# Optimization experiments

Hardware: AMD Instinct MI355X
Metric: run time of the kernel (lower is better)

## Reference

```python
import jax, jax.numpy as jnp
import numpy as np

N = 10000   # num nodes
E = 160000  # num edges (avg degree 16)
B = 8       # batch dim carried on node state
D = 64      # hidden_size


def setup_inputs() -> dict:
    key = jax.random.key(0)
    k1, k2, k3, k4, k5, k6 = jax.random.split(key, 6)
    state = jax.random.normal(k1, (N, B, D), jnp.float32)
    feature = jax.random.normal(k2, (N, 32), jnp.float32)  # unused by GAT math, kept for call signature
    weight = jax.random.normal(k3, (2 * D, D), jnp.float32) * 0.05
    src = jax.random.randint(k4, (E,), 0, N, jnp.int32)
    dst = jax.random.randint(k5, (E,), 0, N, jnp.int32)
    dist = jax.random.uniform(k6, (E, 1), jnp.float32)
    return dict(state=state, feature=feature, weight=weight, src=src, dst=dst, dist=dist)


def reference(state, feature, weight, src, dst, dist):
    # --- msg_edge: gather src/dst node states per edge ---
    src_state = state[src]                 # [E,B,D]
    dst_state = state[dst]                 # [E,B,D]
    es = jnp.concatenate([src_state, dst_state], axis=-1)          # [E,B,2D]
    alpha = jax.nn.leaky_relu(jnp.einsum('ebk,kd->ebd', es, weight),
                              negative_slope=0.2)                  # tf.nn.leaky_relu alpha=0.2
    alpha = alpha * dist[:, :, None]       # dist [E,1] broadcast to [E,1,1]

    # --- msg_reduce: segment softmax over incoming edges of each dst node ---
    amax = jax.ops.segment_max(alpha, dst, num_segments=N)         # [N,B,D]
    ex = jnp.exp(alpha - amax[dst])                                # stable exp
    denom = jax.ops.segment_sum(ex, dst, num_segments=N)           # [N,B,D]
    attn = ex / denom[dst]                                         # [E,B,D]

    # weighted sum of src states scattered back to dst nodes, then relu
    new_state = jax.nn.relu(jax.ops.segment_sum(attn * src_state, dst, num_segments=N))
    return new_state
```

## Files before the change

### kernel.cpp

```cpp
#include <hip/hip_runtime.h>
#include <hip/hip_fp16.h>
#include <math.h>

#define N_NODES 10000
#define N_EDGES 160000
#define B_ 8
#define D_ 64
#define BD 512
#define ROWS 80000
#define SLICE 640000
#define CAP 48

typedef _Float16 f16x8 __attribute__((ext_vector_type(8)));
typedef float f32x4 __attribute__((ext_vector_type(4)));
typedef float f4v __attribute__((ext_vector_type(4)));
typedef unsigned int u32;

union HU { _Float16 f; unsigned short u; };
union HC { u32 u; __half2 h; };

__global__ void __launch_bounds__(256) prep_kernel(
    const int* __restrict__ src, const int* __restrict__ dst,
    const float* __restrict__ dist, int* __restrict__ counts, u32* __restrict__ bucket,
    const float* __restrict__ state, const float* __restrict__ weight,
    __half2* __restrict__ G, __half* __restrict__ Pd) {
    __shared__ _Float16 At[64 * 72];
    __shared__ _Float16 Bt[128 * 72];
    __shared__ u32 Gs[64 * 64];
    __shared__ unsigned short Ps[64 * 64];
    int bid = blockIdx.x;
    int tid = threadIdx.x;

    if (bid < 625) {
        int e = bid * 256 + tid;
        int s = src[e];
        int d = dst[e];
        float di = dist[e];
        int pos = atomicAdd(&counts[d], 1);
        if (pos < CAP) {
            unsigned short hd = __half_as_ushort(__float2half_rn(di * 1.44269504f));
            bucket[d * CAP + pos] = (u32)s | ((u32)hd << 16);
        }
        return;
    }

    int row0 = (bid - 625) * 64;

    const f4v* st4 = (const f4v*)(state + (size_t)row0 * 64);
    for (int i = tid; i < 1024; i += 256) {
        int r = i >> 4, c4 = (i & 15) << 2;
        f4v v = __builtin_nontemporal_load(&st4[i]);
        union { short4 s; _Float16 h[4]; } u;
        u.h[0] = (_Float16)v[0]; u.h[1] = (_Float16)v[1];
        u.h[2] = (_Float16)v[2]; u.h[3] = (_Float16)v[3];
        *(short4*)&At[r * 72 + c4] = u.s;
    }
    const f4v* w4 = (const f4v*)weight;
    for (int i = tid; i < 2048; i += 256) {
        int r = i >> 4, c4 = (i & 15) << 2;
        f4v v = w4[i];
        int h = r >> 6, k = r & 63;
        int nb = h * 64 + c4;
        Bt[(nb + 0) * 72 + k] = (_Float16)v[0];
        Bt[(nb + 1) * 72 + k] = (_Float16)v[1];
        Bt[(nb + 2) * 72 + k] = (_Float16)v[2];
        Bt[(nb + 3) * 72 + k] = (_Float16)v[3];
    }
    __syncthreads();

    int wave = tid >> 6, lane = tid & 63;
    int quad = lane >> 4, m16 = lane & 15;
    int m_loc = wave * 16 + m16;

    f16x8 a0 = *(const f16x8*)&At[m_loc * 72 + quad * 8];
    f16x8 a1 = *(const f16x8*)&At[m_loc * 72 + 32 + quad * 8];

#pragma unroll
    for (int tcol = 0; tcol < 8; tcol++) {
        int n = tcol * 16 + m16;
        f16x8 b0 = *(const f16x8*)&Bt[n * 72 + quad * 8];
        f16x8 b1 = *(const f16x8*)&Bt[n * 72 + 32 + quad * 8];
        f32x4 acc = {0.f, 0.f, 0.f, 0.f};
        acc = __builtin_amdgcn_mfma_f32_16x16x32_f16(a0, b0, acc, 0, 0, 0);
        acc = __builtin_amdgcn_mfma_f32_16x16x32_f16(a1, b1, acc, 0, 0, 0);
#pragma unroll
        for (int r = 0; r < 4; r++) {
            int ml = wave * 16 + quad * 4 + r;
            if (tcol < 4) {
                HU xu; xu.f = At[ml * 72 + n];
                Gs[ml * 64 + n] = (u32)__half_as_ushort(__float2half_rn(acc[r]))
                                  | ((u32)xu.u << 16);
            } else {
                Ps[ml * 64 + (n - 64)] = __half_as_ushort(__float2half_rn(acc[r]));
            }
        }
    }
    __syncthreads();

    for (int i = tid; i < 1024; i += 256) {
        int row = i >> 4, seg = i & 15;
        int m = row0 + row;
        size_t base = (size_t)(m & 7) * SLICE + (size_t)(m >> 3) * 64;
        *(float4*)&G[base + seg * 4] = *(const float4*)&Gs[row * 64 + seg * 4];
    }
    for (int i = tid; i < 512; i += 256) {
        int row = i >> 3, seg = i & 7;
        int m = row0 + row;
        size_t base = (size_t)(m & 7) * SLICE + (size_t)(m >> 3) * 64;
        *(float4*)&Pd[base + seg * 8] = *(const float4*)&Ps[row * 64 + seg * 8];
    }
}

__global__ void __launch_bounds__(256) gat_aggregate(
    const __half2* __restrict__ G,
    const __half* __restrict__ Pds,
    const int* __restrict__ counts,
    const u32* __restrict__ bucket,
    float* __restrict__ out) {
    int bid = blockIdx.x;
    int b = bid & 7;
    int grp = bid >> 3;
    int wave = threadIdx.x >> 6;
    int lane = threadIdx.x & 63;
    int n = (grp << 2) + wave;
    int eidx = lane >> 4;
    int lpart = lane & 15;

    const __half2* Gb = G + (size_t)b * SLICE;
    const __half* Pb = Pds + (size_t)b * SLICE;

    union { double d; __half2 h[2]; } pdu;
    pdu.d = *(const double*)(Pb + n * 64 + lpart * 4);
    __half2 pd01 = pdu.h[0], pd23 = pdu.h[1];

    int cnt = counts[n];
    if (cnt > CAP) cnt = CAP;
    const u32* ep = bucket + n * CAP;

    const __half2 c06 = __float2half2_rn(0.6f);
    const __half2 c04 = __float2half2_rn(0.4f);
    const u32 ABSM = 0x7fff7fffu;

    __half2 l01 = __float2half2_rn(0.f), l23 = l01;
    __half2 o01 = l01, o23 = l01;

    if (cnt > 0) {
        int last = cnt - 1;
        int iA = eidx <= last ? eidx : last;
        int iB = (4 + eidx) <= last ? (4 + eidx) : last;
        u32 recA = ep[iA];
        u32 recB = ep[iB];
        float4 gA = *(const float4*)(Gb + (size_t)(recA & 0xffffu) * 64 + lpart * 4);
        float4 gB = *(const float4*)(Gb + (size_t)(recB & 0xffffu) * 64 + lpart * 4);
        __half hA = __ushort_as_half((unsigned short)(recA >> 16));
        __half hB = __ushort_as_half((unsigned short)(recB >> 16));
        __half2 dA = __halves2half2(hA, hA);
        __half2 dB = __halves2half2(hB, hB);

        int j = 0;
        for (;;) {
            int jn = j + 8;
            bool more = jn < cnt;
            float4 gA2, gB2; __half2 dA2, dB2;
            if (more) {
                int a2 = jn + eidx;      a2 = a2 <= last ? a2 : last;
                int b2 = jn + 4 + eidx;  b2 = b2 <= last ? b2 : last;
                u32 rA2 = ep[a2];
                u32 rB2 = ep[b2];
                gA2 = *(const float4*)(Gb + (size_t)(rA2 & 0xffffu) * 64 + lpart * 4);
                gB2 = *(const float4*)(Gb + (size_t)(rB2 & 0xffffu) * 64 + lpart * 4);
                __half h2a = __ushort_as_half((unsigned short)(rA2 >> 16));
                __half h2b = __ushort_as_half((unsigned short)(rB2 >> 16));
                dA2 = __halves2half2(h2a, h2a);
                dB2 = __halves2half2(h2b, h2b);
            }
#pragma unroll
            for (int c = 0; c < 2; c++) {
                bool act = (j + c * 4 + eidx) <= last;
                float4 g = c == 0 ? gA : gB;
                __half2 ddl = c == 0 ? dA : dB;
                union { float4 f; __half2 h[4]; } gu; gu.f = g;
                __half2 p01 = __halves2half2(__low2half(gu.h[0]), __low2half(gu.h[1]));
                __half2 p23 = __halves2half2(__low2half(gu.h[2]), __low2half(gu.h[3]));
                __half2 x01 = __halves2half2(__high2half(gu.h[0]), __high2half(gu.h[1]));
                __half2 x23 = __halves2half2(__high2half(gu.h[2]), __high2half(gu.h[3]));
                __half2 z01 = __hadd2(p01, pd01);
                __half2 z23 = __hadd2(p23, pd23);
                HC az01, az23, zz01, zz23;
                zz01.h = z01; zz23.h = z23;
                az01.u = zz01.u & ABSM;
                az23.u = zz23.u & ABSM;
                __half2 lk01 = __hfma2(az01.h, c04, __hmul2(z01, c06));
                __half2 lk23 = __hfma2(az23.h, c04, __hmul2(z23, c06));
                __half2 a01 = __hmul2(lk01, ddl);
                __half2 a23 = __hmul2(lk23, ddl);
                __half2 e01 = __halves2half2(hexp2(__low2half(a01)), hexp2(__high2half(a01)));
                __half2 e23 = __halves2half2(hexp2(__low2half(a23)), hexp2(__high2half(a23)));
                HC s01, s23;
                s01.h = e01; s23.h = e23;
                s01.u = act ? s01.u : 0u;
                s23.u = act ? s23.u : 0u;
                l01 = __hadd2(l01, s01.h);
                l23 = __hadd2(l23, s23.h);
                o01 = __hfma2(s01.h, x01, o01);
                o23 = __hfma2(s23.h, x23, o23);
            }
            if (!more) break;
            j = jn; gA = gA2; gB = gB2; dA = dA2; dB = dB2;
        }
#pragma unroll
        for (int m = 16; m <= 32; m <<= 1) {
            HC c;
            c.u = (u32)__shfl_xor((int)((HC){.h = l01}).u, m, 64); l01 = __hadd2(l01, c.h);
            c.u = (u32)__shfl_xor((int)((HC){.h = l23}).u, m, 64); l23 = __hadd2(l23, c.h);
            c.u = (u32)__shfl_xor((int)((HC){.h = o01}).u, m, 64); o01 = __hadd2(o01, c.h);
            c.u = (u32)__shfl_xor((int)((HC){.h = o23}).u, m, 64); o23 = __hadd2(o23, c.h);
        }
    }
    if (eidx == 0) {
        float4 r;
        if (cnt > 0) {
            float l0 = __low2float(l01), l1 = __high2float(l01);
            float l2 = __low2float(l23), l3 = __high2float(l23);
            float o0 = __low2float(o01), o1 = __high2float(o01);
            float o2 = __low2float(o23), o3 = __high2float(o23);
            r.x = fmaxf(o0 * __builtin_amdgcn_rcpf(l0), 0.f);
            r.y = fmaxf(o1 * __builtin_amdgcn_rcpf(l1), 0.f);
            r.z = fmaxf(o2 * __builtin_amdgcn_rcpf(l2), 0.f);
            r.w = fmaxf(o3 * __builtin_amdgcn_rcpf(l3), 0.f);
        } else {
            r = make_float4(0.f, 0.f, 0.f, 0.f);
        }
        *(float4*)(out + (size_t)n * BD + b * 64 + lpart * 4) = r;
    }
}

extern "C" void kernel_launch(void* const* d_in, const int* in_sizes, int n_in,
                              void* d_out, int out_size, void* d_ws, size_t ws_size,
                              hipStream_t stream) {
    const float* state  = (const float*)d_in[0];
    const float* weight = (const float*)d_in[2];
    const int*   src    = (const int*)d_in[3];
    const int*   dst    = (const int*)d_in[4];
    const float* dist   = (const float*)d_in[5];

    __half2* G      = (__half2*)d_ws;
    __half*  Pd     = (__half*)(G + (size_t)8 * SLICE);
    u32*     bucket = (u32*)(Pd + (size_t)8 * SLICE);
    int*     counts = (int*)(bucket + (size_t)N_NODES * CAP);

    hipMemsetAsync(counts, 0, N_NODES * sizeof(int), stream);
    prep_kernel<<<1875, 256, 0, stream>>>(src, dst, dist, counts, bucket,
                                          state, weight, G, Pd);
    gat_aggregate<<<N_NODES * 2, 256, 0, stream>>>(G, Pd, counts, bucket, (float*)d_out);
}
```

Baseline: 155.1 us.

## Pad edge buckets with zero records and repack G as separate p/x half2 pairs

Edge buckets are widened to a padded stride and zeroed by the memset. The aggregate loop now runs over a count rounded up to a multiple of 8, with no per-edge clamping or masking. The padding edges' contribution (node 0, zero dist, so exp=1) is subtracted afterwards. G is also repacked so that the projection halves and the state halves are contiguous half2 pairs, which removes the per-edge shuffling of halves. The cost is a larger memset and an fp16 correction that may lose precision.

```diff
diff --git a/kernel.cpp b/kernel.cpp
--- a/kernel.cpp
+++ b/kernel.cpp
@@ -10,6 +10,7 @@
 #define ROWS 80000
 #define SLICE 640000
 #define CAP 48
+#define CAPR 56
 
 typedef _Float16 f16x8 __attribute__((ext_vector_type(8)));
 typedef float f32x4 __attribute__((ext_vector_type(4)));
@@ -23,10 +24,10 @@
     const int* __restrict__ src, const int* __restrict__ dst,
     const float* __restrict__ dist, int* __restrict__ counts, u32* __restrict__ bucket,
     const float* __restrict__ state, const float* __restrict__ weight,
-    __half2* __restrict__ G, __half* __restrict__ Pd) {
+    u32* __restrict__ G, __half* __restrict__ Pd) {
     __shared__ _Float16 At[64 * 72];
     __shared__ _Float16 Bt[128 * 72];
-    __shared__ u32 Gs[64 * 64];
+    __shared__ unsigned short Ps2[64 * 68];
     __shared__ unsigned short Ps[64 * 64];
     int bid = blockIdx.x;
     int tid = threadIdx.x;
@@ -39,7 +40,7 @@
         int pos = atomicAdd(&counts[d], 1);
         if (pos < CAP) {
             unsigned short hd = __half_as_ushort(__float2half_rn(di * 1.44269504f));
-            bucket[d * CAP + pos] = (u32)s | ((u32)hd << 16);
+            bucket[d * CAPR + pos] = (u32)s | ((u32)hd << 16);
         }
         return;
     }
@@ -86,22 +87,26 @@
 #pragma unroll
         for (int r = 0; r < 4; r++) {
             int ml = wave * 16 + quad * 4 + r;
-            if (tcol < 4) {
-                HU xu; xu.f = At[ml * 72 + n];
-                Gs[ml * 64 + n] = (u32)__half_as_ushort(__float2half_rn(acc[r]))
-                                  | ((u32)xu.u << 16);
-            } else {
-                Ps[ml * 64 + (n - 64)] = __half_as_ushort(__float2half_rn(acc[r]));
-            }
+            unsigned short ph = __half_as_ushort(__float2half_rn(acc[r]));
+            if (tcol < 4) Ps2[ml * 68 + n] = ph;
+            else          Ps[ml * 64 + (n - 64)] = ph;
         }
     }
     __syncthreads();
 
+    const u32* Ps2w = (const u32*)Ps2;
+    const u32* Atw = (const u32*)At;
     for (int i = tid; i < 1024; i += 256) {
-        int row = i >> 4, seg = i & 15;
+        int row = i >> 4, q = i & 15;
         int m = row0 + row;
         size_t base = (size_t)(m & 7) * SLICE + (size_t)(m >> 3) * 64;
-        *(float4*)&G[base + seg * 4] = *(const float4*)&Gs[row * 64 + seg * 4];
+        u32 p01 = Ps2w[row * 34 + q * 2];
+        u32 p23 = Ps2w[row * 34 + q * 2 + 1];
+        u32 x01 = Atw[row * 36 + q * 2];
+        u32 x23 = Atw[row * 36 + q * 2 + 1];
+        float4 v = make_float4(__uint_as_float(p01), __uint_as_float(p23),
+                               __uint_as_float(x01), __uint_as_float(x23));
+        *(float4*)&G[base + q * 4] = v;
     }
     for (int i = tid; i < 512; i += 256) {
         int row = i >> 3, seg = i & 7;
@@ -112,7 +117,7 @@
 }
 
 __global__ void __launch_bounds__(256) gat_aggregate(
-    const __half2* __restrict__ G,
+    const u32* __restrict__ G,
     const __half* __restrict__ Pds,
     const int* __restrict__ counts,
     const u32* __restrict__ bucket,
@@ -126,7 +131,7 @@
     int eidx = lane >> 4;
     int lpart = lane & 15;
 
-    const __half2* Gb = G + (size_t)b * SLICE;
+    const u32* Gb = G + (size_t)b * SLICE;
     const __half* Pb = Pds + (size_t)b * SLICE;
 
     union { double d; __half2 h[2]; } pdu;
@@ -135,7 +140,8 @@
 
     int cnt = counts[n];
     if (cnt > CAP) cnt = CAP;
-    const u32* ep = bucket + n * CAP;
+    int padded = (cnt + 7) & ~7;
+    const u32* ep = bucket + n * CAPR;
 
     const __half2 c06 = __float2half2_rn(0.6f);
     const __half2 c04 = __float2half2_rn(0.4f);
@@ -144,12 +150,9 @@
     __half2 l01 = __float2half2_rn(0.f), l23 = l01;
     __half2 o01 = l01, o23 = l01;
 
-    if (cnt > 0) {
-        int last = cnt - 1;
-        int iA = eidx <= last ? eidx : last;
-        int iB = (4 + eidx) <= last ? (4 + eidx) : last;
-        u32 recA = ep[iA];
-        u32 recB = ep[iB];
+    if (padded > 0) {
+        u32 recA = ep[eidx];
+        u32 recB = ep[4 + eidx];
         float4 gA = *(const float4*)(Gb + (size_t)(recA & 0xffffu) * 64 + lpart * 4);
         float4 gB = *(const float4*)(Gb + (size_t)(recB & 0xffffu) * 64 + lpart * 4);
         __half hA = __ushort_as_half((unsigned short)(recA >> 16));
@@ -160,13 +163,11 @@
         int j = 0;
         for (;;) {
             int jn = j + 8;
-            bool more = jn < cnt;
+            bool more = jn < padded;
             float4 gA2, gB2; __half2 dA2, dB2;
             if (more) {
-                int a2 = jn + eidx;      a2 = a2 <= last ? a2 : last;
-                int b2 = jn + 4 + eidx;  b2 = b2 <= last ? b2 : last;
-                u32 rA2 = ep[a2];
-                u32 rB2 = ep[b2];
+                u32 rA2 = ep[jn + eidx];
+                u32 rB2 = ep[jn + 4 + eidx];
                 gA2 = *(const float4*)(Gb + (size_t)(rA2 & 0xffffu) * 64 + lpart * 4);
                 gB2 = *(const float4*)(Gb + (size_t)(rB2 & 0xffffu) * 64 + lpart * 4);
                 __half h2a = __ushort_as_half((unsigned short)(rA2 >> 16));
@@ -176,14 +177,11 @@
             }
 #pragma unroll
             for (int c = 0; c < 2; c++) {
-                bool act = (j + c * 4 + eidx) <= last;
                 float4 g = c == 0 ? gA : gB;
                 __half2 ddl = c == 0 ? dA : dB;
                 union { float4 f; __half2 h[4]; } gu; gu.f = g;
-                __half2 p01 = __halves2half2(__low2half(gu.h[0]), __low2half(gu.h[1]));
-                __half2 p23 = __halves2half2(__low2half(gu.h[2]), __low2half(gu.h[3]));
-                __half2 x01 = __halves2half2(__high2half(gu.h[0]), __high2half(gu.h[1]));
-                __half2 x23 = __halves2half2(__high2half(gu.h[2]), __high2half(gu.h[3]));
+                __half2 p01 = gu.h[0], p23 = gu.h[1];
+                __half2 x01 = gu.h[2], x23 = gu.h[3];
                 __half2 z01 = __hadd2(p01, pd01);
                 __half2 z23 = __hadd2(p23, pd23);
                 HC az01, az23, zz01, zz23;
@@ -196,14 +194,10 @@
                 __half2 a23 = __hmul2(lk23, ddl);
                 __half2 e01 = __halves2half2(hexp2(__low2half(a01)), hexp2(__high2half(a01)));
                 __half2 e23 = __halves2half2(hexp2(__low2half(a23)), hexp2(__high2half(a23)));
-                HC s01, s23;
-                s01.h = e01; s23.h = e23;
-                s01.u = act ? s01.u : 0u;
-                s23.u = act ? s23.u : 0u;
-                l01 = __hadd2(l01, s01.h);
-                l23 = __hadd2(l23, s23.h);
-                o01 = __hfma2(s01.h, x01, o01);
-                o23 = __hfma2(s23.h, x23, o23);
+                l01 = __hadd2(l01, e01);
+                l23 = __hadd2(l23, e23);
+                o01 = __hfma2(e01, x01, o01);
+                o23 = __hfma2(e23, x23, o23);
             }
             if (!more) break;
             j = jn; gA = gA2; gB = gB2; dA = dA2; dB = dB2;
@@ -215,6 +209,17 @@
             c.u = (u32)__shfl_xor((int)((HC){.h = l23}).u, m, 64); l23 = __hadd2(l23, c.h);
             c.u = (u32)__shfl_xor((int)((HC){.h = o01}).u, m, 64); o01 = __hadd2(o01, c.h);
             c.u = (u32)__shfl_xor((int)((HC){.h = o23}).u, m, 64); o23 = __hadd2(o23, c.h);
+        }
+        int npads = padded - cnt;
+        if (npads) {
+            float4 g0 = *(const float4*)(Gb + lpart * 4);
+            union { float4 f; __half2 h[4]; } g0u; g0u.f = g0;
+            __half2 np = __float2half2_rn((float)npads);
+            l01 = __hsub2(l01, np);
+            l23 = __hsub2(l23, np);
+            __half2 nneg = __hneg2(np);
+            o01 = __hfma2(nneg, g0u.h[2], o01);
+            o23 = __hfma2(nneg, g0u.h[3], o23);
         }
     }
     if (eidx == 0) {
@@ -244,12 +249,12 @@
     const int*   dst    = (const int*)d_in[4];
     const float* dist   = (const float*)d_in[5];
 
-    __half2* G      = (__half2*)d_ws;
-    __half*  Pd     = (__half*)(G + (size_t)8 * SLICE);
-    u32*     bucket = (u32*)(Pd + (size_t)8 * SLICE);
-    int*     counts = (int*)(bucket + (size_t)N_NODES * CAP);
-
-    hipMemsetAsync(counts, 0, N_NODES * sizeof(int), stream);
+    u32*    G      = (u32*)d_ws;
+    __half* Pd     = (__half*)(G + (size_t)8 * SLICE);
+    u32*    bucket = (u32*)(Pd + (size_t)8 * SLICE);
+    int*    counts = (int*)(bucket + (size_t)N_NODES * CAPR);
+
+    hipMemsetAsync(bucket, 0, ((size_t)N_NODES * CAPR + N_NODES) * sizeof(u32), stream);
     prep_kernel<<<1875, 256, 0, stream>>>(src, dst, dist, counts, bucket,
                                           state, weight, G, Pd);
     gat_aggregate<<<N_NODES * 2, 256, 0, stream>>>(G, Pd, counts, bucket, (float*)d_out);
```

Measured after the change: 148.8 us. 1.04x faster.
